# Performance work log

Measured on AMD Instinct MI355X. Metric: run time of the kernel, lower is better.

The kernel has to match this reference:

```python
import jax, jax.numpy as jnp
import numpy as np

EPS = 1e-8  # matches F.cosine_similarity default eps
N_CLASSES = 10


def _mlp(x, W1, b1, W2, b2):
    # Embedding MLP: Linear -> ReLU -> Linear (dims=[64,128,64])
    h = jax.nn.relu(x @ W1 + b1)
    return h @ W2 + b2


def setup_inputs() -> dict:
    key = jax.random.key(0)
    ks = jax.random.split(key, 5)
    d_in, d_hid, d_out = 64, 128, 64
    B_test, B_train = 8192, 16384
    X = jax.random.normal(ks[0], (B_test, d_in), dtype=jnp.float32)
    x_train = jax.random.normal(ks[1], (B_train, d_in), dtype=jnp.float32)
    y_train = jax.random.randint(ks[2], (B_train,), 0, N_CLASSES)
    W1 = jax.random.normal(ks[3], (d_in, d_hid), dtype=jnp.float32) * (1.0 / np.sqrt(d_in))
    b1 = jnp.zeros((d_hid,), dtype=jnp.float32)
    W2 = jax.random.normal(ks[4], (d_hid, d_out), dtype=jnp.float32) * (1.0 / np.sqrt(d_hid))
    b2 = jnp.zeros((d_out,), dtype=jnp.float32)
    return {"X": X, "x_train": x_train, "y_train": y_train,
            "W1": W1, "b1": b1, "W2": W2, "b2": b2}


def reference(X, x_train, y_train, W1, b1, W2, b2):
    test_embd = _mlp(X, W1, b1, W2, b2)          # [B_test, d]
    train_embd = _mlp(x_train, W1, b1, W2, b2)   # [B_train, d]
    # Cosine similarity between every (test, train) pair, vectorized.
    # F.cosine_similarity: dot / max(||a||*||b||, eps)
    dots = test_embd @ train_embd.T                       # [B_test, B_train]
    tn = jnp.linalg.norm(test_embd, axis=1, keepdims=True)   # [B_test, 1]
    sn = jnp.linalg.norm(train_embd, axis=1, keepdims=True)  # [B_train, 1]
    sims = dots / jnp.maximum(tn * sn.T, EPS)
    proba = jax.nn.softmax(sims, axis=1)                  # attention over train set
    one_hot = jax.nn.one_hot(y_train, N_CLASSES, dtype=proba.dtype)  # [B_train, C]
    # Weighted one-hot vote: replaces the per-row Python loop with a matmul.
    preds = proba @ one_hot                               # [B_test, C]
    return preds
```

## Files before the change

kernel.cpp:

```cpp
#include <hip/hip_runtime.h>
#include <hip/hip_bf16.h>


typedef __attribute__((ext_vector_type(8))) _Float16 half8;
typedef __attribute__((ext_vector_type(2))) __fp16 fp16x2;
typedef __attribute__((ext_vector_type(4))) float floatx4;
typedef unsigned short u16;
typedef unsigned int u32;

#define LOG2E 1.4426950408889634f
#define TS 16

__global__ __launch_bounds__(256) void k_prep(
    const float* __restrict__ W1, const float* __restrict__ W2,
    const int* __restrict__ y, u16* __restrict__ W1f, u16* __restrict__ W2f,
    u16* __restrict__ Vf, float* __restrict__ acc)
{
    const int tid16 = blockIdx.x * 256 + threadIdx.x;

    {
        const int e0   = tid16 * 16;
        const int f32  = e0 >> 9;
        const int l0   = (e0 >> 3) & 63;
        const int quad = l0 >> 4;
        const int n0   = l0 & 15;
        int yv[8];
        #pragma unroll
        for (int r = 0; r < 4; r++) {
            yv[r]     = y[f32 * 32 + quad * 4 + r];
            yv[4 + r] = y[f32 * 32 + 16 + quad * 4 + r];
        }
        half8 v0, v1;
        #pragma unroll
        for (int j = 0; j < 8; j++) {
            v0[j] = (n0     == yv[j] || n0     == 10) ? (_Float16)1.0f : (_Float16)0.0f;
            v1[j] = (n0 + 1 == yv[j] || n0 + 1 == 10) ? (_Float16)1.0f : (_Float16)0.0f;
        }
        *(half8*)(Vf + e0)     = v0;
        *(half8*)(Vf + e0 + 8) = v1;
    }

    {
        const int idx = tid16;
        if (idx < 8192) {
            int e = idx, fid = e >> 9, l = (e >> 3) & 63, jj = e & 7;
            int n1 = (fid >> 1) * 16 + (l & 15);
            int k1 = (fid & 1) * 32 + (l >> 4) * 8 + jj;
            ((_Float16*)W1f)[e] = (_Float16)W1[k1 * 128 + n1];
        } else {
            int e = idx - 8192, fid = e >> 9, l = (e >> 3) & 63, jj = e & 7;
            int n2 = (fid >> 2) * 16 + (l & 15);
            int k2 = (fid & 3) * 32 + (l >> 4) * 8 + jj;
            ((_Float16*)W2f)[e] = (_Float16)W2[k2 * 64 + n2];
        }
    }

    {
        floatx4 z = {0.f, 0.f, 0.f, 0.f};
        floatx4* p = (floatx4*)(acc + tid16 * 8);
        p[0] = z; p[1] = z;
    }
}

#define HSTR 136

__global__ __launch_bounds__(256) void k_embed(
    const float* __restrict__ X, const float* __restrict__ Xtr,
    const u16* __restrict__ W1f, const float* __restrict__ b1,
    const u16* __restrict__ W2f, const float* __restrict__ b2,
    u16* __restrict__ Etf, u16* __restrict__ Etrf)
{
    __shared__ __align__(16) _Float16 Hbuf[4][16][HSTR];
    const int w = threadIdx.x >> 6, lane = threadIdx.x & 63;
    const int m = lane & 15, g = lane >> 4;
    const int strip = blockIdx.x * 4 + w;
    const int row0  = strip * 16;
    const bool isTest = (row0 < 8192);
    const float* src = isTest ? (X + (size_t)row0 * 64)
                              : (Xtr + (size_t)(row0 - 8192) * 64);
    const floatx4 fz = {0.f, 0.f, 0.f, 0.f};

    const float* prow = src + m * 64;
    half8 a0, a1;
    {
        floatx4 x0 = *(const floatx4*)(prow + g * 8);
        floatx4 x1 = *(const floatx4*)(prow + g * 8 + 4);
        floatx4 x2 = *(const floatx4*)(prow + 32 + g * 8);
        floatx4 x3 = *(const floatx4*)(prow + 32 + g * 8 + 4);
        #pragma unroll
        for (int j = 0; j < 4; j++) {
            a0[j] = (_Float16)x0[j]; a0[4 + j] = (_Float16)x1[j];
            a1[j] = (_Float16)x2[j]; a1[4 + j] = (_Float16)x3[j];
        }
    }

    #pragma unroll
    for (int nt = 0; nt < 8; nt++) {
        half8 bw0 = *(const half8*)(W1f + (nt * 2 + 0) * 512 + lane * 8);
        half8 bw1 = *(const half8*)(W1f + (nt * 2 + 1) * 512 + lane * 8);
        floatx4 acc = __builtin_amdgcn_mfma_f32_16x16x32_f16(a0, bw0, fz, 0, 0, 0);
        acc = __builtin_amdgcn_mfma_f32_16x16x32_f16(a1, bw1, acc, 0, 0, 0);
        float bias = b1[nt * 16 + m];
        #pragma unroll
        for (int r = 0; r < 4; r++) {
            float h = acc[r] + bias;
            h = h > 0.f ? h : 0.f;
            Hbuf[w][g * 4 + r][nt * 16 + m] = (_Float16)h;
        }
    }

    half8 ha[4];
    #pragma unroll
    for (int kt = 0; kt < 4; kt++)
        ha[kt] = *(const half8*)(&Hbuf[w][m][kt * 32 + g * 8]);

    float ef[4][4];
    #pragma unroll
    for (int nt = 0; nt < 4; nt++) {
        floatx4 acc = fz;
        #pragma unroll
        for (int kt = 0; kt < 4; kt++) {
            half8 bw = *(const half8*)(W2f + (nt * 4 + kt) * 512 + lane * 8);
            acc = __builtin_amdgcn_mfma_f32_16x16x32_f16(ha[kt], bw, acc, 0, 0, 0);
        }
        float bias = b2[nt * 16 + m];
        #pragma unroll
        for (int r = 0; r < 4; r++) ef[nt][r] = acc[r] + bias;
    }

    const float sc = isTest ? LOG2E : 1.0f;
    float rn[4];
    #pragma unroll
    for (int r = 0; r < 4; r++) {
        float ss = 0.f;
        #pragma unroll
        for (int nt = 0; nt < 4; nt++) ss += ef[nt][r] * ef[nt][r];
        ss += __shfl_xor(ss, 1);
        ss += __shfl_xor(ss, 2);
        ss += __shfl_xor(ss, 4);
        ss += __shfl_xor(ss, 8);
        rn[r] = rsqrtf(fmaxf(ss, 1e-30f)) * sc;
    }

    u16* dst = isTest ? Etf : Etrf;
    const int stile = (isTest ? row0 : row0 - 8192) >> 4;
    #pragma unroll
    for (int nt = 0; nt < 4; nt++) {
        int col = nt * 16 + m;
        int kt = col >> 5, gg = (col >> 3) & 3, jj = col & 7;
        #pragma unroll
        for (int r = 0; r < 4; r++) {
            int rloc = g * 4 + r;
            ((_Float16*)dst)[(stile * 2 + kt) * 512 + (gg * 16 + rloc) * 8 + jj] =
                (_Float16)(ef[nt][r] * rn[r]);
        }
    }
}

__global__ __launch_bounds__(256, 3) void k_main(
    const u16* __restrict__ Etf, const u16* __restrict__ Etrf,
    const u16* __restrict__ Vf, float* __restrict__ acc)
{
    __shared__ float Obuf[4][128][16];
    const int w = threadIdx.x >> 6, lane = threadIdx.x & 63;
    const int m = lane & 15, g = lane >> 4;
    const int bx = blockIdx.x, by = blockIdx.y;
    const floatx4 fz = {0.f, 0.f, 0.f, 0.f};

    half8 b[8][2];
    #pragma unroll
    for (int ns = 0; ns < 8; ns++) {
        int stile = bx * 8 + ns;
        b[ns][0] = *(const half8*)(Etf + (stile * 2 + 0) * 512 + lane * 8);
        b[ns][1] = *(const half8*)(Etf + (stile * 2 + 1) * 512 + lane * 8);
    }

    floatx4 o[8] = {fz, fz, fz, fz, fz, fz, fz, fz};
    const int wstart = by * 1024 + w * 256;

    const u16* e0p = Etrf + (size_t)(wstart >> 3) * 512 + lane * 8;
    half8 a0 = *(const half8*)(e0p);
    half8 a1 = *(const half8*)(e0p + 512);
    half8 a2 = *(const half8*)(e0p + 1024);
    half8 a3 = *(const half8*)(e0p + 1536);
    half8 vf = *(const half8*)(Vf + (size_t)(wstart >> 5) * 512 + lane * 8);

    for (int g32 = 0; g32 < 8; g32++) {
        const int gn  = (g32 < 7) ? g32 + 1 : 7;
        const int t32n = wstart + gn * 32;
        const u16* enp = Etrf + (size_t)(t32n >> 3) * 512 + lane * 8;
        half8 na0 = *(const half8*)(enp);
        half8 na1 = *(const half8*)(enp + 512);
        half8 na2 = *(const half8*)(enp + 1024);
        half8 na3 = *(const half8*)(enp + 1536);
        half8 nvf = *(const half8*)(Vf + (size_t)(t32n >> 5) * 512 + lane * 8);

        #pragma unroll
        for (int ns = 0; ns < 8; ns++) {
            floatx4 s0 = __builtin_amdgcn_mfma_f32_16x16x32_f16(a0, b[ns][0], fz, 0, 0, 0);
            s0 = __builtin_amdgcn_mfma_f32_16x16x32_f16(a1, b[ns][1], s0, 0, 0, 0);
            floatx4 s1 = __builtin_amdgcn_mfma_f32_16x16x32_f16(a2, b[ns][0], fz, 0, 0, 0);
            s1 = __builtin_amdgcn_mfma_f32_16x16x32_f16(a3, b[ns][1], s1, 0, 0, 0);
            float p0 = __builtin_amdgcn_exp2f(s0[0]);
            float p1 = __builtin_amdgcn_exp2f(s0[1]);
            float p2 = __builtin_amdgcn_exp2f(s0[2]);
            float p3 = __builtin_amdgcn_exp2f(s0[3]);
            float p4 = __builtin_amdgcn_exp2f(s1[0]);
            float p5 = __builtin_amdgcn_exp2f(s1[1]);
            float p6 = __builtin_amdgcn_exp2f(s1[2]);
            float p7 = __builtin_amdgcn_exp2f(s1[3]);
            union { fp16x2 h2[4]; half8 h8; } P;
            P.h2[0] = __builtin_amdgcn_cvt_pkrtz(p0, p1);
            P.h2[1] = __builtin_amdgcn_cvt_pkrtz(p2, p3);
            P.h2[2] = __builtin_amdgcn_cvt_pkrtz(p4, p5);
            P.h2[3] = __builtin_amdgcn_cvt_pkrtz(p6, p7);
            o[ns] = __builtin_amdgcn_mfma_f32_16x16x32_f16(P.h8, vf, o[ns], 0, 0, 0);
        }
        a0 = na0; a1 = na1; a2 = na2; a3 = na3; vf = nvf;
    }

    #pragma unroll
    for (int ms = 0; ms < 8; ms++)
        #pragma unroll
        for (int r = 0; r < 4; r++)
            Obuf[w][ms * 16 + g * 4 + r][m] = o[ms][r];
    __syncthreads();
    for (int i = threadIdx.x; i < 2048; i += 256) {
        int mm = i >> 4, c = i & 15;
        float s = Obuf[0][mm][c] + Obuf[1][mm][c] + Obuf[2][mm][c] + Obuf[3][mm][c];
        atomicAdd(&acc[(bx * 128 + mm) * 16 + c], s);
    }
}

__global__ __launch_bounds__(256) void k_final(
    const float* __restrict__ acc, float* __restrict__ out)
{
    int row = blockIdx.x * 256 + threadIdx.x;
    if (row < 8192) {
        const floatx4* src = (const floatx4*)(acc + (size_t)row * 16);
        floatx4 s0 = src[0], s1 = src[1], s2 = src[2];
        float inv = 1.0f / s2[2];
        out[row * 10 + 0] = s0[0] * inv;
        out[row * 10 + 1] = s0[1] * inv;
        out[row * 10 + 2] = s0[2] * inv;
        out[row * 10 + 3] = s0[3] * inv;
        out[row * 10 + 4] = s1[0] * inv;
        out[row * 10 + 5] = s1[1] * inv;
        out[row * 10 + 6] = s1[2] * inv;
        out[row * 10 + 7] = s1[3] * inv;
        out[row * 10 + 8] = s2[0] * inv;
        out[row * 10 + 9] = s2[1] * inv;
    }
}

extern "C" void kernel_launch(void* const* d_in, const int* in_sizes, int n_in,
                              void* d_out, int out_size, void* d_ws, size_t ws_size,
                              hipStream_t stream)
{
    const float* X   = (const float*)d_in[0];
    const float* Xtr = (const float*)d_in[1];
    const int*   y   = (const int*)d_in[2];
    const float* W1  = (const float*)d_in[3];
    const float* b1  = (const float*)d_in[4];
    const float* W2  = (const float*)d_in[5];
    const float* b2  = (const float*)d_in[6];
    float* out = (float*)d_out;

    char* ws = (char*)d_ws;
    float* acc = (float*)ws;
    u16* Etf  = (u16*)(ws + 524288);
    u16* Etrf = (u16*)(ws + 524288 + 1048576);
    u16* Vf   = (u16*)(ws + 524288 + 1048576 + 2097152);
    u16* W1f  = (u16*)(ws + 524288 + 1048576 + 2097152 + 524288);
    u16* W2f  = W1f + 8192;

    k_prep<<<64, 256, 0, stream>>>(W1, W2, y, W1f, W2f, Vf, acc);
    k_embed<<<384, 256, 0, stream>>>(X, Xtr, W1f, b1, W2f, b2, Etf, Etrf);
    k_main<<<dim3(64, TS), 256, 0, stream>>>(Etf, Etrf, Vf, acc);
    k_final<<<32, 256, 0, stream>>>(acc, out);
}
```

Baseline: 100.4 us.

## Fold prep into embed kernel and replace atomics with per-split partial buffers

Measured after the change: 101.6 us. No clear change (+1.2%).

```diff
diff --git a/kernel.cpp b/kernel.cpp
--- a/kernel.cpp
+++ b/kernel.cpp
@@ -11,15 +11,19 @@
 #define LOG2E 1.4426950408889634f
 #define TS 16
 
-__global__ __launch_bounds__(256) void k_prep(
-    const float* __restrict__ W1, const float* __restrict__ W2,
-    const int* __restrict__ y, u16* __restrict__ W1f, u16* __restrict__ W2f,
-    u16* __restrict__ Vf, float* __restrict__ acc)
-{
-    const int tid16 = blockIdx.x * 256 + threadIdx.x;
-
-    {
-        const int e0   = tid16 * 16;
+#define HSTR 136
+
+__global__ __launch_bounds__(256) void k_embed(
+    const float* __restrict__ X, const float* __restrict__ Xtr,
+    const float* __restrict__ W1, const float* __restrict__ b1,
+    const float* __restrict__ W2, const float* __restrict__ b2,
+    const int* __restrict__ y,
+    u16* __restrict__ Etf, u16* __restrict__ Etrf, u16* __restrict__ Vf)
+{
+    const int bx = blockIdx.x;
+
+    if (bx >= 384) {
+        const int e0   = ((bx - 384) * 256 + threadIdx.x) * 16;
         const int f32  = e0 >> 9;
         const int l0   = (e0 >> 3) & 63;
         const int quad = l0 >> 4;
@@ -38,42 +42,39 @@
         }
         *(half8*)(Vf + e0)     = v0;
         *(half8*)(Vf + e0 + 8) = v1;
-    }
+        return;
+    }
+
+    __shared__ __align__(16) _Float16 W1L[8192];
+    __shared__ __align__(16) _Float16 W2L[8192];
+    __shared__ __align__(16) _Float16 Hbuf[4][16][HSTR];
+    __shared__ __align__(16) _Float16 Ebuf[4][1024];
 
     {
-        const int idx = tid16;
-        if (idx < 8192) {
-            int e = idx, fid = e >> 9, l = (e >> 3) & 63, jj = e & 7;
-            int n1 = (fid >> 1) * 16 + (l & 15);
-            int k1 = (fid & 1) * 32 + (l >> 4) * 8 + jj;
-            ((_Float16*)W1f)[e] = (_Float16)W1[k1 * 128 + n1];
-        } else {
-            int e = idx - 8192, fid = e >> 9, l = (e >> 3) & 63, jj = e & 7;
-            int n2 = (fid >> 2) * 16 + (l & 15);
-            int k2 = (fid & 3) * 32 + (l >> 4) * 8 + jj;
-            ((_Float16*)W2f)[e] = (_Float16)W2[k2 * 64 + n2];
-        }
-    }
-
-    {
-        floatx4 z = {0.f, 0.f, 0.f, 0.f};
-        floatx4* p = (floatx4*)(acc + tid16 * 8);
-        p[0] = z; p[1] = z;
-    }
-}
-
-#define HSTR 136
-
-__global__ __launch_bounds__(256) void k_embed(
-    const float* __restrict__ X, const float* __restrict__ Xtr,
-    const u16* __restrict__ W1f, const float* __restrict__ b1,
-    const u16* __restrict__ W2f, const float* __restrict__ b2,
-    u16* __restrict__ Etf, u16* __restrict__ Etrf)
-{
-    __shared__ __align__(16) _Float16 Hbuf[4][16][HSTR];
+        const int t = threadIdx.x;
+        #pragma unroll
+        for (int i8 = 0; i8 < 4; i8++) {
+            half8 v1, v2;
+            #pragma unroll
+            for (int j = 0; j < 8; j++) {
+                int e = t * 32 + i8 * 8 + j;
+                int fid = e >> 9, l = (e >> 3) & 63, jj = e & 7;
+                int n1 = (fid >> 1) * 16 + (l & 15);
+                int k1 = (fid & 1) * 32 + (l >> 4) * 8 + jj;
+                v1[j] = (_Float16)W1[k1 * 128 + n1];
+                int n2 = (fid >> 2) * 16 + (l & 15);
+                int k2 = (fid & 3) * 32 + (l >> 4) * 8 + jj;
+                v2[j] = (_Float16)W2[k2 * 64 + n2];
+            }
+            *(half8*)&W1L[t * 32 + i8 * 8] = v1;
+            *(half8*)&W2L[t * 32 + i8 * 8] = v2;
+        }
+    }
+    __syncthreads();
+
     const int w = threadIdx.x >> 6, lane = threadIdx.x & 63;
     const int m = lane & 15, g = lane >> 4;
-    const int strip = blockIdx.x * 4 + w;
+    const int strip = bx * 4 + w;
     const int row0  = strip * 16;
     const bool isTest = (row0 < 8192);
     const float* src = isTest ? (X + (size_t)row0 * 64)
@@ -96,8 +97,8 @@
 
     #pragma unroll
     for (int nt = 0; nt < 8; nt++) {
-        half8 bw0 = *(const half8*)(W1f + (nt * 2 + 0) * 512 + lane * 8);
-        half8 bw1 = *(const half8*)(W1f + (nt * 2 + 1) * 512 + lane * 8);
+        half8 bw0 = *(const half8*)&W1L[(nt * 2 + 0) * 512 + lane * 8];
+        half8 bw1 = *(const half8*)&W1L[(nt * 2 + 1) * 512 + lane * 8];
         floatx4 acc = __builtin_amdgcn_mfma_f32_16x16x32_f16(a0, bw0, fz, 0, 0, 0);
         acc = __builtin_amdgcn_mfma_f32_16x16x32_f16(a1, bw1, acc, 0, 0, 0);
         float bias = b1[nt * 16 + m];
@@ -120,7 +121,7 @@
         floatx4 acc = fz;
         #pragma unroll
         for (int kt = 0; kt < 4; kt++) {
-            half8 bw = *(const half8*)(W2f + (nt * 4 + kt) * 512 + lane * 8);
+            half8 bw = *(const half8*)&W2L[(nt * 4 + kt) * 512 + lane * 8];
             acc = __builtin_amdgcn_mfma_f32_16x16x32_f16(ha[kt], bw, acc, 0, 0, 0);
         }
         float bias = b2[nt * 16 + m];
@@ -142,8 +143,6 @@
         rn[r] = rsqrtf(fmaxf(ss, 1e-30f)) * sc;
     }
 
-    u16* dst = isTest ? Etf : Etrf;
-    const int stile = (isTest ? row0 : row0 - 8192) >> 4;
     #pragma unroll
     for (int nt = 0; nt < 4; nt++) {
         int col = nt * 16 + m;
@@ -151,15 +150,22 @@
         #pragma unroll
         for (int r = 0; r < 4; r++) {
             int rloc = g * 4 + r;
-            ((_Float16*)dst)[(stile * 2 + kt) * 512 + (gg * 16 + rloc) * 8 + jj] =
+            Ebuf[w][kt * 512 + (gg * 16 + rloc) * 8 + jj] =
                 (_Float16)(ef[nt][r] * rn[r]);
         }
+    }
+    u16* dst = isTest ? Etf : Etrf;
+    const int stile = (isTest ? row0 : row0 - 8192) >> 4;
+    #pragma unroll
+    for (int kt = 0; kt < 2; kt++) {
+        half8 ev = *(const half8*)&Ebuf[w][kt * 512 + lane * 8];
+        *(half8*)((_Float16*)dst + (size_t)(stile * 2 + kt) * 512 + lane * 8) = ev;
     }
 }
 
 __global__ __launch_bounds__(256, 3) void k_main(
     const u16* __restrict__ Etf, const u16* __restrict__ Etrf,
-    const u16* __restrict__ Vf, float* __restrict__ acc)
+    const u16* __restrict__ Vf, float* __restrict__ accp)
 {
     __shared__ float Obuf[4][128][16];
     const int w = threadIdx.x >> 6, lane = threadIdx.x & 63;
@@ -228,17 +234,21 @@
     for (int i = threadIdx.x; i < 2048; i += 256) {
         int mm = i >> 4, c = i & 15;
         float s = Obuf[0][mm][c] + Obuf[1][mm][c] + Obuf[2][mm][c] + Obuf[3][mm][c];
-        atomicAdd(&acc[(bx * 128 + mm) * 16 + c], s);
+        accp[((size_t)by * 8192 + bx * 128 + mm) * 16 + c] = s;
     }
 }
 
 __global__ __launch_bounds__(256) void k_final(
-    const float* __restrict__ acc, float* __restrict__ out)
+    const float* __restrict__ accp, float* __restrict__ out)
 {
     int row = blockIdx.x * 256 + threadIdx.x;
     if (row < 8192) {
-        const floatx4* src = (const floatx4*)(acc + (size_t)row * 16);
-        floatx4 s0 = src[0], s1 = src[1], s2 = src[2];
+        floatx4 s0 = {0.f,0.f,0.f,0.f}, s1 = s0, s2 = s0;
+        #pragma unroll
+        for (int p = 0; p < TS; p++) {
+            const floatx4* src = (const floatx4*)(accp + ((size_t)p * 8192 + row) * 16);
+            s0 += src[0]; s1 += src[1]; s2 += src[2];
+        }
         float inv = 1.0f / s2[2];
         out[row * 10 + 0] = s0[0] * inv;
         out[row * 10 + 1] = s0[1] * inv;
@@ -267,15 +277,12 @@
     float* out = (float*)d_out;
 
     char* ws = (char*)d_ws;
-    float* acc = (float*)ws;
-    u16* Etf  = (u16*)(ws + 524288);
-    u16* Etrf = (u16*)(ws + 524288 + 1048576);
-    u16* Vf   = (u16*)(ws + 524288 + 1048576 + 2097152);
-    u16* W1f  = (u16*)(ws + 524288 + 1048576 + 2097152 + 524288);
-    u16* W2f  = W1f + 8192;
-
-    k_prep<<<64, 256, 0, stream>>>(W1, W2, y, W1f, W2f, Vf, acc);
-    k_embed<<<384, 256, 0, stream>>>(X, Xtr, W1f, b1, W2f, b2, Etf, Etrf);
-    k_main<<<dim3(64, TS), 256, 0, stream>>>(Etf, Etrf, Vf, acc);
-    k_final<<<32, 256, 0, stream>>>(acc, out);
-}
+    float* accp = (float*)ws;
+    u16* Etf  = (u16*)(ws + 8388608);
+    u16* Etrf = (u16*)(ws + 8388608 + 1048576);
+    u16* Vf   = (u16*)(ws + 8388608 + 1048576 + 2097152);
+
+    k_embed<<<448, 256, 0, stream>>>(X, Xtr, W1, b1, W2, b2, y, Etf, Etrf, Vf);
+    k_main<<<dim3(64, TS), 256, 0, stream>>>(Etf, Etrf, Vf, accp);
+    k_final<<<32, 256, 0, stream>>>(accp, out);
+}
```
